# Kernel optimization log

Measured on AMD Instinct MI355X. Metric: run time of the kernel, lower is better.

Reference implementation:

```python
import jax, jax.numpy as jnp
import numpy as np

N = 20000      # nodes
E = 320000     # edges (avg degree 16)
DIN, H1, H2, DOUT = 256, 256, 128, 64


def _lin_params(key, din, dout):
    kw, kb = jax.random.split(key)
    s = 1.0 / np.sqrt(din)
    W = jax.random.uniform(kw, (din, dout), jnp.float32, -s, s)
    b = jax.random.uniform(kb, (dout,), jnp.float32, -s, s)
    return W, b


def setup_inputs() -> dict:
    key = jax.random.key(0)
    keys = jax.random.split(key, 20)
    inp = {
        'x': jax.random.normal(keys[0], (N, DIN), jnp.float32),
        'edge_index': jax.random.randint(keys[1], (2, E), 0, N, jnp.int64),
    }
    dims = [(DIN, H1), (DIN, H1), (DIN, H1),   # layer1 key/query/value
            (H1, H2), (H1, H2), (H1, H2),      # layer2
            (H2, DOUT), (H2, DOUT), (H2, DOUT)]  # layer3
    names = ['k1', 'q1', 'v1', 'k2', 'q2', 'v2', 'k3', 'q3', 'v3']
    for i, (nm, (di, do)) in enumerate(zip(names, dims)):
        W, b = _lin_params(keys[2 + i], di, do)
        inp[nm + '_w'] = W
        inp[nm + '_b'] = b
    # skip (root) weights, no bias per PyG, plus per-conv output bias
    for j, (di, do) in enumerate([(DIN, H1), (H1, H2), (H2, DOUT)], start=1):
        s = 1.0 / np.sqrt(di)
        inp[f's{j}_w'] = jax.random.uniform(keys[11 + 2 * j], (di, do), jnp.float32, -s, s)
        inp[f'bias{j}'] = jnp.zeros((do,), jnp.float32)
    return inp


def _res_gated_conv(x, src, dst, kw, kb, qw, qb, vw, vb, sw, bias):
    # PyG ResGatedGraphConv (flow source_to_target, aggr='add', act=Sigmoid):
    # out_i = lin_skip(x_i) + sum_{j->i} sigmoid(lin_key(x_i) + lin_query(x_j)) * lin_value(x_j) + bias
    k = x @ kw + kb            # [N, D]
    q = x @ qw + qb
    v = x @ vw + vb
    eta = jax.nn.sigmoid(k[dst] + q[src])   # [E, D] edge gate
    msg = eta * v[src]                      # [E, D]
    agg = jax.ops.segment_sum(msg, dst, num_segments=N)  # scatter-add to targets
    return x @ sw + agg + bias


def reference(x, edge_index,
              k1_w, k1_b, q1_w, q1_b, v1_w, v1_b,
              k2_w, k2_b, q2_w, q2_b, v2_w, v2_b,
              k3_w, k3_b, q3_w, q3_b, v3_w, v3_b,
              s1_w, bias1, s2_w, bias2, s3_w, bias3):
    src, dst = edge_index[0], edge_index[1]
    h = _res_gated_conv(x, src, dst, k1_w, k1_b, q1_w, q1_b, v1_w, v1_b, s1_w, bias1)
    # dropout (eval mode -> identity)
    h = _res_gated_conv(h, src, dst, k2_w, k2_b, q2_w, q2_b, v2_w, v2_b, s2_w, bias2)
    h = _res_gated_conv(h, src, dst, k3_w, k3_b, q3_w, q3_b, v3_w, v3_b, s3_w, bias3)
    return jax.nn.softmax(h, axis=1)
```

## Files before the change

### kernel.cpp

```cpp
#include <hip/hip_runtime.h>
#include <hip/hip_bf16.h>
#include <type_traits>


#define NN 20000
#define EE 320000
#define ELLW 64

typedef _Float16 half8 __attribute__((ext_vector_type(8)));
typedef _Float16 half4 __attribute__((ext_vector_type(4)));
typedef _Float16 half2v __attribute__((ext_vector_type(2)));
typedef float f32x4 __attribute__((ext_vector_type(4)));

__device__ __forceinline__ _Float16 f2h(float f) { return (_Float16)f; }
__device__ __forceinline__ float fsigmoid_mul(float v, float x) {
    return v * __builtin_amdgcn_rcpf(1.f + __expf(-x));
}

struct PrepArgs {
    const float* w[3][4];
    const float* b[3][4];
    _Float16* wt[3];
    float* cb[3];
};

__global__ __launch_bounds__(256) void setup_all_kernel(
    const int* __restrict__ ei, int* __restrict__ deg, int* __restrict__ flag,
    const float* __restrict__ x, _Float16* __restrict__ Xh, PrepArgs a) {
    const int b = blockIdx.x;
    const int tid = threadIdx.x;
    if (b < 79) {
        const int i = b * 256 + tid;
        if (i < NN) deg[i] = 0;
    } else if (b == 79) {
        __shared__ int nz;
        if (tid == 0) nz = 0;
        __syncthreads();
        int c = 0;
        for (int t = tid; t < 1024; t += 256)
            if (ei[2 * t + 1] != 0) c = 1;
        if (c) atomicAdd(&nz, 1);
        __syncthreads();
        if (tid == 0) *flag = (nz == 0) ? 1 : 0;
    } else if (b < 1744) {
        const int idx = (b - 80) * 256 + tid;
        int layer, li, K, D, s;
        if (idx < 262144) {
            layer = 0; li = idx; K = 256; D = 256; s = 2;
        } else if (idx < 393216) {
            layer = 1; li = idx - 262144; K = 256; D = 128; s = 1;
        } else {
            layer = 2; li = idx - 393216; K = 128; D = 64; s = 0;
        }
        const int p = li / K;
        const int k = li - p * K;
        const int DV = D >> 6;
        int grp, c;
        if (p < D) {
            grp = 0; c = p;
        } else if (p < 3 * D) {
            const int t = p - D;
            const int g = t >> (s + 1);
            const int r = t & (2 * DV - 1);
            if (r < DV) { grp = 1; c = g * DV + r; }
            else        { grp = 2; c = g * DV + r - DV; }
        } else {
            grp = 3; c = p - 3 * D;
        }
        a.wt[layer][(size_t)p * K + k] =
            f2h(a.w[layer][grp][(size_t)k * D + c]);
        if (k == 0) a.cb[layer][p] = a.b[layer][grp][c];
    } else {
        const int i = ((b - 1744) * 256 + tid) * 8;
        if (i < NN * 256) {
            const float4 f0 = *(const float4*)(x + i);
            const float4 f1 = *(const float4*)(x + i + 4);
            half8 h;
            h[0] = f2h(f0.x); h[1] = f2h(f0.y); h[2] = f2h(f0.z); h[3] = f2h(f0.w);
            h[4] = f2h(f1.x); h[5] = f2h(f1.y); h[6] = f2h(f1.z); h[7] = f2h(f1.w);
            *(half8*)(Xh + i) = h;
        }
    }
}

__device__ __forceinline__ void gemm_tile(
    int bm, int bn, const _Float16* __restrict__ A,
    const _Float16* __restrict__ Bt, const float* __restrict__ catbias,
    _Float16* __restrict__ O, int M, int K, int N) {
    __shared__ _Float16 As[2][4096];
    __shared__ _Float16 Bs[2][4096];

    const int tid = threadIdx.x;
    const int wid = tid >> 6;
    const int lane = tid & 63;
    const int tile_m = bm * 128;
    const int tile_n = bn * 128;
    const int wm = (wid & 1) * 64;
    const int wn = (wid >> 1) * 64;

    const int st_row = (wid << 4) + (lane >> 2);
    const int st_kc = (lane & 3) << 3;

    auto stage = [&](int buf, int kt) {
#pragma unroll
        for (int j = 0; j < 2; ++j) {
            int ar = tile_m + j * 64 + st_row;
            ar = ar < M ? ar : M - 1;
            const _Float16* ag = A + (size_t)ar * K + kt + st_kc;
            __builtin_amdgcn_global_load_lds(
                (const __attribute__((address_space(1))) unsigned int*)ag,
                (__attribute__((address_space(3))) unsigned int*)
                    &As[buf][j * 2048 + (wid << 9)],
                16, 0, 0);
            const int br = tile_n + j * 64 + st_row;
            const _Float16* bg = Bt + (size_t)br * K + kt + st_kc;
            __builtin_amdgcn_global_load_lds(
                (const __attribute__((address_space(1))) unsigned int*)bg,
                (__attribute__((address_space(3))) unsigned int*)
                    &Bs[buf][j * 2048 + (wid << 9)],
                16, 0, 0);
        }
    };

    stage(0, 0);

    f32x4 acc[4][4] = {};
    const int fr = lane & 15;
    const int fk = (lane >> 4) << 3;
    const int niter = K >> 5;

    for (int it = 0; it < niter; ++it) {
        __syncthreads();
        if (it + 1 < niter) stage((it + 1) & 1, (it + 1) << 5);
        const _Float16* as = As[it & 1];
        const _Float16* bs = Bs[it & 1];
        half8 af[4], bf[4];
#pragma unroll
        for (int mi = 0; mi < 4; ++mi)
            af[mi] = *(const half8*)&as[(wm + mi * 16 + fr) * 32 + fk];
#pragma unroll
        for (int ni = 0; ni < 4; ++ni)
            bf[ni] = *(const half8*)&bs[(wn + ni * 16 + fr) * 32 + fk];
#pragma unroll
        for (int mi = 0; mi < 4; ++mi)
#pragma unroll
            for (int ni = 0; ni < 4; ++ni)
                acc[mi][ni] = __builtin_amdgcn_mfma_f32_16x16x32_f16(
                    af[mi], bf[ni], acc[mi][ni], 0, 0, 0);
    }
    __syncthreads();

    _Float16* zone = &As[0][0] + wid * 2048;
    const int cl = lane & 15;
    const int rq = (lane >> 4) << 2;
    const int col0 = tile_n + wn;
    const int r0 = tile_m + wm;
#pragma unroll
    for (int mi = 0; mi < 4; ++mi) {
#pragma unroll
        for (int ni = 0; ni < 4; ++ni) {
            const float cb = catbias[col0 + ni * 16 + cl];
#pragma unroll
            for (int r = 0; r < 4; ++r)
                zone[(rq + r) * 72 + ni * 16 + cl] = f2h(acc[mi][ni][r] + cb);
        }
#pragma unroll
        for (int j = 0; j < 2; ++j) {
            const int rr = j * 8 + (lane >> 3);
            const int row = r0 + mi * 16 + rr;
            const half8 v = *(const half8*)&zone[rr * 72 + (lane & 7) * 8];
            if (row < M)
                *(half8*)&O[(size_t)row * N + col0 + (lane & 7) * 8] = v;
        }
    }
}

__global__ __launch_bounds__(256) void gemm_kernel(
    const _Float16* __restrict__ A, const _Float16* __restrict__ Bt,
    const float* __restrict__ catbias, _Float16* __restrict__ O, int M, int K,
    int N, int mblocks) {
    gemm_tile(blockIdx.x % mblocks, blockIdx.x / mblocks, A, Bt, catbias, O, M,
              K, N);
}

__global__ __launch_bounds__(256) void gemm1_fill_kernel(
    const _Float16* __restrict__ A, const _Float16* __restrict__ Bt,
    const float* __restrict__ catbias, _Float16* __restrict__ O,
    const int* __restrict__ ei, const int* __restrict__ i64flag,
    int* __restrict__ deg, int* __restrict__ col) {
    if (blockIdx.x < 1256) {
        gemm_tile(blockIdx.x % 157, blockIdx.x / 157, A, Bt, catbias, O, NN,
                  256, 1024);
        return;
    }
    const int e = (blockIdx.x - 1256) * 256 + threadIdx.x;
    if (e >= EE) return;
    int src, dst;
    if (*i64flag) {
        const long long* p = (const long long*)ei;
        src = (int)p[e];
        dst = (int)p[EE + e];
    } else {
        src = ei[e];
        dst = ei[EE + e];
    }
    const int pos = atomicAdd(&deg[dst], 1);
    if (pos < ELLW) col[dst * ELLW + pos] = src;
}

template <int D, int MODE>
__global__ __launch_bounds__(256, 4) void edge_gather_kernel(
    const int* __restrict__ deg, const int* __restrict__ col,
    const _Float16* __restrict__ KQVS, _Float16* __restrict__ Hh,
    float* __restrict__ out, int n) {
    constexpr int DV = D / 64;
    constexpr int D4 = 4 * D;
    using qv_t = typename std::conditional<
        DV == 4, half8,
        typename std::conditional<DV == 2, half4, half2v>::type>::type;

    const int node = blockIdx.x * 4 + (threadIdx.x >> 6);
    if (node >= n) return;
    const int lane = threadIdx.x & 63;
    const int ld = lane * DV;

    int dg = deg[node];
    dg = dg < ELLW ? dg : ELLW;
    int idx = col[node * ELLW + lane];
    if (lane >= dg) idx = node;

    float k[DV], acc[DV];
    {
        const _Float16* kp = KQVS + (size_t)node * D4 + ld;
        if constexpr (DV == 4) {
            const half4 u = *(const half4*)kp;
#pragma unroll
            for (int j = 0; j < 4; ++j) k[j] = (float)u[j];
        } else if constexpr (DV == 2) {
            const half2v u = *(const half2v*)kp;
            k[0] = (float)u[0]; k[1] = (float)u[1];
        } else {
            k[0] = (float)*kp;
        }
    }
#pragma unroll
    for (int j = 0; j < DV; ++j) acc[j] = 0.f;

    auto ldqv = [&](qv_t& u, int e) {
        const int s = __builtin_amdgcn_readlane(idx, e);
        const qv_t* p = (const qv_t*)(KQVS + (size_t)s * D4 + D) + lane;
        u = *p;
    };
    auto edgeacc = [&](qv_t u) {
#pragma unroll
        for (int j = 0; j < DV; ++j)
            acc[j] += fsigmoid_mul((float)u[DV + j], k[j] + (float)u[j]);
    };

    qv_t ua[8], ub[8];
    auto issue = [&](qv_t* u, int e0) {
#pragma unroll
        for (int j = 0; j < 8; ++j) ldqv(u[j], e0 + j);
    };
    auto consume8 = [&](qv_t* u) {
#pragma unroll
        for (int j = 0; j < 8; ++j) edgeacc(u[j]);
    };
    auto consume_tail = [&](qv_t* u, int nb) {
#pragma unroll
        for (int j = 0; j < 8; ++j)
            if (j < nb) edgeacc(u[j]);
    };

    if (dg > 0) {
        issue(ua, 0);
        for (int e = 0;;) {
            int nb = dg - e;
            if (nb <= 8) {
                __builtin_amdgcn_sched_barrier(0);
                consume_tail(ua, nb);
                break;
            }
            issue(ub, e + 8);
            __builtin_amdgcn_sched_barrier(0);
            consume8(ua);
            e += 8;
            nb = dg - e;
            if (nb <= 8) {
                __builtin_amdgcn_sched_barrier(0);
                consume_tail(ub, nb);
                break;
            }
            issue(ua, e + 8);
            __builtin_amdgcn_sched_barrier(0);
            consume8(ub);
            e += 8;
        }
    }

    float h[DV];
    {
        const _Float16* sp = KQVS + (size_t)node * D4 + 3 * D + ld;
        if constexpr (DV == 4) {
            const half4 u = *(const half4*)sp;
#pragma unroll
            for (int j = 0; j < 4; ++j) h[j] = (float)u[j] + acc[j];
        } else if constexpr (DV == 2) {
            const half2v u = *(const half2v*)sp;
            h[0] = (float)u[0] + acc[0];
            h[1] = (float)u[1] + acc[1];
        } else {
            h[0] = (float)*sp + acc[0];
        }
    }

    if constexpr (MODE == 0) {
        _Float16* op = Hh + (size_t)node * D + ld;
        if constexpr (DV == 4) {
            half4 o;
#pragma unroll
            for (int j = 0; j < 4; ++j) o[j] = f2h(h[j]);
            *(half4*)op = o;
        } else if constexpr (DV == 2) {
            half2v o;
            o[0] = f2h(h[0]); o[1] = f2h(h[1]);
            *(half2v*)op = o;
        } else {
            op[0] = f2h(h[0]);
        }
    } else {
        static_assert(MODE == 0 || DV == 1, "softmax fusion needs D==64");
        float m = h[0];
#pragma unroll
        for (int off = 32; off > 0; off >>= 1)
            m = fmaxf(m, __shfl_xor(m, off, 64));
        const float ex = __expf(h[0] - m);
        float sm = ex;
#pragma unroll
        for (int off = 32; off > 0; off >>= 1) sm += __shfl_xor(sm, off, 64);
        out[(size_t)node * 64 + lane] = ex * __builtin_amdgcn_rcpf(sm);
    }
}

extern "C" void kernel_launch(void* const* d_in, const int* in_sizes, int n_in,
                              void* d_out, int out_size, void* d_ws,
                              size_t ws_size, hipStream_t stream) {
    const float* x = (const float*)d_in[0];
    const int* ei = (const int*)d_in[1];

    char* w = (char*)d_ws;
    _Float16* Xh = (_Float16*)w;     w += (size_t)NN * 256 * 2;
    _Float16* KQVS = (_Float16*)w;   w += (size_t)NN * 1024 * 2;
    _Float16* H1h = (_Float16*)w;    w += (size_t)NN * 256 * 2;
    _Float16* H2h = (_Float16*)w;    w += (size_t)NN * 128 * 2;
    _Float16* Wt1 = (_Float16*)w;    w += (size_t)1024 * 256 * 2;
    _Float16* Wt2 = (_Float16*)w;    w += (size_t)512 * 256 * 2;
    _Float16* Wt3 = (_Float16*)w;    w += (size_t)256 * 128 * 2;
    float* cb1 = (float*)w;          w += 1024 * 4;
    float* cb2 = (float*)w;          w += 512 * 4;
    float* cb3 = (float*)w;          w += 256 * 4;
    int* i64flag = (int*)w;          w += 16;
    int* deg = (int*)w;              w += (size_t)NN * 4;
    int* ell = (int*)w;              w += (size_t)NN * ELLW * 4;

    const dim3 blk(256);
    const int gblocks = (NN + 3) / 4;

    PrepArgs pa;
    pa.w[0][0] = (const float*)d_in[2];  pa.b[0][0] = (const float*)d_in[3];
    pa.w[0][1] = (const float*)d_in[4];  pa.b[0][1] = (const float*)d_in[5];
    pa.w[0][2] = (const float*)d_in[6];  pa.b[0][2] = (const float*)d_in[7];
    pa.w[1][0] = (const float*)d_in[8];  pa.b[1][0] = (const float*)d_in[9];
    pa.w[1][1] = (const float*)d_in[10]; pa.b[1][1] = (const float*)d_in[11];
    pa.w[1][2] = (const float*)d_in[12]; pa.b[1][2] = (const float*)d_in[13];
    pa.w[2][0] = (const float*)d_in[14]; pa.b[2][0] = (const float*)d_in[15];
    pa.w[2][1] = (const float*)d_in[16]; pa.b[2][1] = (const float*)d_in[17];
    pa.w[2][2] = (const float*)d_in[18]; pa.b[2][2] = (const float*)d_in[19];
    pa.w[0][3] = (const float*)d_in[20]; pa.b[0][3] = (const float*)d_in[21];
    pa.w[1][3] = (const float*)d_in[22]; pa.b[1][3] = (const float*)d_in[23];
    pa.w[2][3] = (const float*)d_in[24]; pa.b[2][3] = (const float*)d_in[25];
    pa.wt[0] = Wt1; pa.wt[1] = Wt2; pa.wt[2] = Wt3;
    pa.cb[0] = cb1; pa.cb[1] = cb2; pa.cb[2] = cb3;

    setup_all_kernel<<<4244, blk, 0, stream>>>(ei, deg, i64flag, x, Xh, pa);

    gemm1_fill_kernel<<<2506, blk, 0, stream>>>(Xh, Wt1, cb1, KQVS, ei,
                                                i64flag, deg, ell);
    edge_gather_kernel<256, 0><<<gblocks, blk, 0, stream>>>(
        deg, ell, KQVS, H1h, nullptr, NN);

    gemm_kernel<<<157 * 4, blk, 0, stream>>>(H1h, Wt2, cb2, KQVS, NN, 256, 512,
                                             157);
    edge_gather_kernel<128, 0><<<gblocks, blk, 0, stream>>>(
        deg, ell, KQVS, H2h, nullptr, NN);

    gemm_kernel<<<157 * 2, blk, 0, stream>>>(H2h, Wt3, cb3, KQVS, NN, 128, 256,
                                             157);
    edge_gather_kernel<64, 1><<<gblocks, blk, 0, stream>>>(
        deg, ell, KQVS, nullptr, (float*)d_out, NN);
}
```

Baseline: 256.7 us.

## Slice feature dimension across blocks in edge gather and shrink ELL indices to 16-bit

Layers 1 and 2 now use a new gather kernel that splits the feature dimension into 32-wide slices handled by separate blocks, with two edges processed per wavefront half. The idea is to shrink each block's working set in KQVS so neighbor rows stay cache-resident, and to raise parallelism. The Q/V weight columns are re-interleaved as pairs so each lane reads one half2 holding both values. ELL column indices are stored as 16-bit, which halves index traffic but only holds because node indices fit in 16 bits (N=20000). The sliced design issues many more small loads and reads deg/col once per slice.

```diff
diff --git a/kernel.cpp b/kernel.cpp
--- a/kernel.cpp
+++ b/kernel.cpp
@@ -44,26 +44,23 @@
         if (tid == 0) *flag = (nz == 0) ? 1 : 0;
     } else if (b < 1744) {
         const int idx = (b - 80) * 256 + tid;
-        int layer, li, K, D, s;
+        int layer, li, K, D;
         if (idx < 262144) {
-            layer = 0; li = idx; K = 256; D = 256; s = 2;
+            layer = 0; li = idx; K = 256; D = 256;
         } else if (idx < 393216) {
-            layer = 1; li = idx - 262144; K = 256; D = 128; s = 1;
+            layer = 1; li = idx - 262144; K = 256; D = 128;
         } else {
-            layer = 2; li = idx - 393216; K = 128; D = 64; s = 0;
+            layer = 2; li = idx - 393216; K = 128; D = 64;
         }
         const int p = li / K;
         const int k = li - p * K;
-        const int DV = D >> 6;
         int grp, c;
         if (p < D) {
             grp = 0; c = p;
         } else if (p < 3 * D) {
             const int t = p - D;
-            const int g = t >> (s + 1);
-            const int r = t & (2 * DV - 1);
-            if (r < DV) { grp = 1; c = g * DV + r; }
-            else        { grp = 2; c = g * DV + r - DV; }
+            grp = (t & 1) ? 2 : 1;
+            c = t >> 1;
         } else {
             grp = 3; c = p - 3 * D;
         }
@@ -187,7 +184,7 @@
     const _Float16* __restrict__ A, const _Float16* __restrict__ Bt,
     const float* __restrict__ catbias, _Float16* __restrict__ O,
     const int* __restrict__ ei, const int* __restrict__ i64flag,
-    int* __restrict__ deg, int* __restrict__ col) {
+    int* __restrict__ deg, unsigned short* __restrict__ col) {
     if (blockIdx.x < 1256) {
         gemm_tile(blockIdx.x % 157, blockIdx.x / 157, A, Bt, catbias, O, NN,
                   256, 1024);
@@ -205,12 +202,55 @@
         dst = ei[EE + e];
     }
     const int pos = atomicAdd(&deg[dst], 1);
-    if (pos < ELLW) col[dst * ELLW + pos] = src;
+    if (pos < ELLW) col[dst * ELLW + pos] = (unsigned short)src;
+}
+
+template <int D>
+__global__ __launch_bounds__(256) void edge_gather_slice_kernel(
+    const int* __restrict__ deg, const unsigned short* __restrict__ col,
+    const _Float16* __restrict__ KQVS, _Float16* __restrict__ Hh, int n) {
+    constexpr int NSL = D / 32;
+    constexpr int D4 = 4 * D;
+    const int b = blockIdx.x;
+    const int s = b % NSL;
+    const int g = b / NSL;
+    const int node = g * 4 + (threadIdx.x >> 6);
+    if (node >= n) return;
+    const int lane = threadIdx.x & 63;
+    const int d = lane & 31;
+    const int esub = lane >> 5;
+
+    int dg = deg[node];
+    dg = dg < ELLW ? dg : ELLW;
+    int idx = (int)col[node * ELLW + lane];
+    if (lane >= dg) idx = node;
+
+    const int el = s * 32 + d;
+    const float k = (float)KQVS[(size_t)node * D4 + el];
+    const _Float16* qv = KQVS + D + 2 * el;
+    float acc = 0.f;
+
+    for (int e = 0; e < dg; e += 4) {
+        const int s0 = __shfl(idx, e + esub, 64);
+        const int s1 = __shfl(idx, e + 2 + esub, 64);
+        const half2v u0 = *(const half2v*)(qv + (size_t)s0 * D4);
+        const half2v u1 = *(const half2v*)(qv + (size_t)s1 * D4);
+        const float g0 = fsigmoid_mul((float)u0[1], k + (float)u0[0]);
+        acc += (e + esub < dg) ? g0 : 0.f;
+        const float g1 = fsigmoid_mul((float)u1[1], k + (float)u1[0]);
+        acc += (e + 2 + esub < dg) ? g1 : 0.f;
+    }
+    acc += __shfl_xor(acc, 32, 64);
+
+    if (lane < 32) {
+        const float skip = (float)KQVS[(size_t)node * D4 + 3 * D + el];
+        Hh[(size_t)node * D + el] = f2h(skip + acc);
+    }
 }
 
 template <int D, int MODE>
 __global__ __launch_bounds__(256, 4) void edge_gather_kernel(
-    const int* __restrict__ deg, const int* __restrict__ col,
+    const int* __restrict__ deg, const unsigned short* __restrict__ col,
     const _Float16* __restrict__ KQVS, _Float16* __restrict__ Hh,
     float* __restrict__ out, int n) {
     constexpr int DV = D / 64;
@@ -226,7 +266,7 @@
 
     int dg = deg[node];
     dg = dg < ELLW ? dg : ELLW;
-    int idx = col[node * ELLW + lane];
+    int idx = (int)col[node * ELLW + lane];
     if (lane >= dg) idx = node;
 
     float k[DV], acc[DV];
@@ -254,7 +294,7 @@
     auto edgeacc = [&](qv_t u) {
 #pragma unroll
         for (int j = 0; j < DV; ++j)
-            acc[j] += fsigmoid_mul((float)u[DV + j], k[j] + (float)u[j]);
+            acc[j] += fsigmoid_mul((float)u[2 * j + 1], k[j] + (float)u[2 * j]);
     };
 
     qv_t ua[8], ub[8];
@@ -361,7 +401,7 @@
     float* cb3 = (float*)w;          w += 256 * 4;
     int* i64flag = (int*)w;          w += 16;
     int* deg = (int*)w;              w += (size_t)NN * 4;
-    int* ell = (int*)w;              w += (size_t)NN * ELLW * 4;
+    unsigned short* ell = (unsigned short*)w;  w += (size_t)NN * ELLW * 2;
 
     const dim3 blk(256);
     const int gblocks = (NN + 3) / 4;
@@ -386,13 +426,13 @@
 
     gemm1_fill_kernel<<<2506, blk, 0, stream>>>(Xh, Wt1, cb1, KQVS, ei,
                                                 i64flag, deg, ell);
-    edge_gather_kernel<256, 0><<<gblocks, blk, 0, stream>>>(
-        deg, ell, KQVS, H1h, nullptr, NN);
+    edge_gather_slice_kernel<256><<<gblocks * 8, blk, 0, stream>>>(
+        deg, ell, KQVS, H1h, NN);
 
     gemm_kernel<<<157 * 4, blk, 0, stream>>>(H1h, Wt2, cb2, KQVS, NN, 256, 512,
                                              157);
-    edge_gather_kernel<128, 0><<<gblocks, blk, 0, stream>>>(
-        deg, ell, KQVS, H2h, nullptr, NN);
+    edge_gather_slice_kernel<128><<<gblocks * 4, blk, 0, stream>>>(
+        deg, ell, KQVS, H2h, NN);
 
     gemm_kernel<<<157 * 2, blk, 0, stream>>>(H2h, Wt3, cb3, KQVS, NN, 128, 256,
                                              157);
```

After: 287.2 us. 11.9% more time.

## Process two edges per wavefront in layer-2/3 gather with double-buffered loads

Applied to the files above, without the earlier changes.

Adds a new edge-gather kernel for D=128 and D=64. Each 64-lane wavefront splits into two half-waves that handle alternate edges, so every lane stays busy even when the feature width is narrower than the wavefront. Loads for the next 8 edges are issued before the current 8 are consumed, with ping-pong buffers and schedule barriers to overlap memory latency. Partial sums from the two halves are combined with a cross-half shuffle, and softmax is done across 32 lanes. The cost is more registers and slightly more complex tail masking.

```diff
diff --git a/kernel.cpp b/kernel.cpp
--- a/kernel.cpp
+++ b/kernel.cpp
@@ -329,7 +329,6 @@
             op[0] = f2h(h[0]);
         }
     } else {
-        static_assert(MODE == 0 || DV == 1, "softmax fusion needs D==64");
         float m = h[0];
 #pragma unroll
         for (int off = 32; off > 0; off >>= 1)
@@ -339,6 +338,146 @@
 #pragma unroll
         for (int off = 32; off > 0; off >>= 1) sm += __shfl_xor(sm, off, 64);
         out[(size_t)node * 64 + lane] = ex * __builtin_amdgcn_rcpf(sm);
+    }
+}
+
+template <int D, int MODE>
+__global__ __launch_bounds__(256, 4) void edge_gather2_kernel(
+    const int* __restrict__ deg, const int* __restrict__ col,
+    const _Float16* __restrict__ KQVS, _Float16* __restrict__ Hh,
+    float* __restrict__ out, int n) {
+    static_assert(D == 64 || D == 128, "edge_gather2 supports D=64/128");
+    constexpr int D4 = 4 * D;
+    constexpr int F = D / 32;
+    using qv_t = typename std::conditional<D == 128, half8, half4>::type;
+
+    const int node = blockIdx.x * 4 + (threadIdx.x >> 6);
+    if (node >= n) return;
+    const int lane = threadIdx.x & 63;
+    const int fl = lane & 31;
+    const int eh = lane >> 5;
+
+    int dg = deg[node];
+    dg = dg < ELLW ? dg : ELLW;
+    int idx = col[node * ELLW + lane];
+    if (lane >= dg) idx = node;
+
+    float k[F], acc[F];
+#pragma unroll
+    for (int j = 0; j < F; ++j) acc[j] = 0.f;
+    {
+        const _Float16* kp = KQVS + (size_t)node * D4 + fl * F;
+        if constexpr (F == 4) {
+            const half4 u = *(const half4*)kp;
+#pragma unroll
+            for (int j = 0; j < 4; ++j) k[j] = (float)u[j];
+        } else {
+            const half2v u = *(const half2v*)kp;
+            k[0] = (float)u[0]; k[1] = (float)u[1];
+        }
+    }
+
+    auto ldqv = [&](qv_t& u, int e2) {
+        const int sA = __builtin_amdgcn_readlane(idx, e2);
+        const int sB = __builtin_amdgcn_readlane(idx, e2 + 1);
+        const int s = (lane < 32) ? sA : sB;
+        u = *((const qv_t*)(KQVS + (size_t)s * D4 + D) + fl);
+    };
+    auto edgeacc = [&](qv_t u, float m) {
+        if constexpr (D == 128) {
+            acc[0] += m * fsigmoid_mul((float)u[2], k[0] + (float)u[0]);
+            acc[1] += m * fsigmoid_mul((float)u[3], k[1] + (float)u[1]);
+            acc[2] += m * fsigmoid_mul((float)u[6], k[2] + (float)u[4]);
+            acc[3] += m * fsigmoid_mul((float)u[7], k[3] + (float)u[5]);
+        } else {
+            acc[0] += m * fsigmoid_mul((float)u[1], k[0] + (float)u[0]);
+            acc[1] += m * fsigmoid_mul((float)u[3], k[1] + (float)u[2]);
+        }
+    };
+
+    qv_t ua[4], ub[4];
+    auto issue = [&](qv_t* u, int e0) {
+#pragma unroll
+        for (int i = 0; i < 4; ++i) ldqv(u[i], e0 + 2 * i);
+    };
+    auto consume4 = [&](qv_t* u) {
+#pragma unroll
+        for (int i = 0; i < 4; ++i) edgeacc(u[i], 1.f);
+    };
+    auto consume_tail = [&](qv_t* u, int nb) {
+#pragma unroll
+        for (int i = 0; i < 4; ++i) {
+            const float m = (2 * i + eh < nb) ? 1.f : 0.f;
+            edgeacc(u[i], m);
+        }
+    };
+
+    if (dg > 0) {
+        issue(ua, 0);
+        for (int e = 0;;) {
+            int nb = dg - e;
+            if (nb <= 8) {
+                __builtin_amdgcn_sched_barrier(0);
+                consume_tail(ua, nb);
+                break;
+            }
+            issue(ub, e + 8);
+            __builtin_amdgcn_sched_barrier(0);
+            consume4(ua);
+            e += 8;
+            nb = dg - e;
+            if (nb <= 8) {
+                __builtin_amdgcn_sched_barrier(0);
+                consume_tail(ub, nb);
+                break;
+            }
+            issue(ua, e + 8);
+            __builtin_amdgcn_sched_barrier(0);
+            consume4(ub);
+            e += 8;
+        }
+    }
+
+#pragma unroll
+    for (int j = 0; j < F; ++j) acc[j] += __shfl_xor(acc[j], 32, 64);
+
+    float h[F];
+    {
+        const _Float16* sp = KQVS + (size_t)node * D4 + 3 * D + fl * F;
+        if constexpr (F == 4) {
+            const half4 u = *(const half4*)sp;
+#pragma unroll
+            for (int j = 0; j < 4; ++j) h[j] = (float)u[j] + acc[j];
+        } else {
+            const half2v u = *(const half2v*)sp;
+            h[0] = (float)u[0] + acc[0];
+            h[1] = (float)u[1] + acc[1];
+        }
+    }
+
+    if constexpr (MODE == 0) {
+        if (lane < 32) {
+            half4 o;
+#pragma unroll
+            for (int j = 0; j < 4; ++j) o[j] = f2h(h[j]);
+            *(half4*)(Hh + (size_t)node * D + fl * F) = o;
+        }
+    } else {
+        static_assert(MODE == 0 || D == 64, "softmax fusion needs D==64");
+        float m = fmaxf(h[0], h[1]);
+#pragma unroll
+        for (int off = 1; off <= 16; off <<= 1)
+            m = fmaxf(m, __shfl_xor(m, off, 64));
+        const float e0 = __expf(h[0] - m);
+        const float e1 = __expf(h[1] - m);
+        float sm = e0 + e1;
+#pragma unroll
+        for (int off = 1; off <= 16; off <<= 1) sm += __shfl_xor(sm, off, 64);
+        if (lane < 32) {
+            const float r = __builtin_amdgcn_rcpf(sm);
+            float2 o = {e0 * r, e1 * r};
+            *(float2*)(out + (size_t)node * 64 + fl * 2) = o;
+        }
     }
 }
 
@@ -391,11 +530,11 @@
 
     gemm_kernel<<<157 * 4, blk, 0, stream>>>(H1h, Wt2, cb2, KQVS, NN, 256, 512,
                                              157);
-    edge_gather_kernel<128, 0><<<gblocks, blk, 0, stream>>>(
+    edge_gather2_kernel<128, 0><<<gblocks, blk, 0, stream>>>(
         deg, ell, KQVS, H2h, nullptr, NN);
 
     gemm_kernel<<<157 * 2, blk, 0, stream>>>(H2h, Wt3, cb3, KQVS, NN, 128, 256,
                                              157);
-    edge_gather_kernel<64, 1><<<gblocks, blk, 0, stream>>>(
+    edge_gather2_kernel<64, 1><<<gblocks, blk, 0, stream>>>(
         deg, ell, KQVS, nullptr, (float*)d_out, NN);
 }
```

After: 266.4 us. +3.8%, slower.
